# Performance work log

Hardware: AMD Instinct MI355X
Metric: run time of the kernel (lower is better)

## Reference

```python
import jax, jax.numpy as jnp
import numpy as np
from jax import lax

CONF_THRESH = 0.65
NMS_THRESH = 0.55
EPS = 1e-16


def setup_inputs() -> dict:
    key = jax.random.key(0)
    x = jax.random.uniform(key, (8, 4096, 85), dtype=jnp.float32)
    return {"x": x}


def _xywh2xyxy(b):
    # b: [..., 4] center-x, center-y, w, h -> x1, y1, x2, y2
    cx, cy, w, h = b[..., 0], b[..., 1], b[..., 2], b[..., 3]
    return jnp.stack([cx - w / 2, cy - h / 2, cx + w / 2, cy + h / 2], axis=-1)


def _pairwise_iou(boxes):
    # boxes: [bs, N, 4] in xyxy -> iou: [bs, N, N]
    x1, y1, x2, y2 = boxes[..., 0], boxes[..., 1], boxes[..., 2], boxes[..., 3]
    ix1 = jnp.maximum(x1[:, :, None], x1[:, None, :])
    iy1 = jnp.maximum(y1[:, :, None], y1[:, None, :])
    ix2 = jnp.minimum(x2[:, :, None], x2[:, None, :])
    iy2 = jnp.minimum(y2[:, :, None], y2[:, None, :])
    inter = jnp.clip(ix2 - ix1, 0.0) * jnp.clip(iy2 - iy1, 0.0)
    area = (x2 - x1) * (y2 - y1)
    return inter / (area[:, :, None] + area[:, None, :] - inter + EPS)


def reference(x):
    # x: [bs, N, 5 + nC]
    bs, N, _ = x.shape
    obj = x[..., 4]
    valid = obj > CONF_THRESH                      # foreground filter
    boxes = _xywh2xyxy(x[..., :4])
    max_conf = jnp.max(x[..., 5:], axis=-1)        # per-box best class score
    cls_idx = jnp.argmax(x[..., 5:], axis=-1)

    # sort descending by class confidence (invalid boxes pushed to the end)
    sort_key = jnp.where(valid, max_conf, -jnp.inf)
    order = jnp.argsort(-sort_key, axis=1)         # [bs, N]
    boxes_s = jnp.take_along_axis(boxes, order[..., None], axis=1)
    obj_s = jnp.take_along_axis(obj, order, axis=1)
    conf_s = jnp.take_along_axis(max_conf, order, axis=1)
    cls_s = jnp.take_along_axis(cls_idx, order, axis=1)
    valid_s = jnp.take_along_axis(valid, order, axis=1)

    # candidate suppression matrix: same class AND IoU above threshold
    iou = _pairwise_iou(boxes_s)                   # [bs, N, N]
    same_cls = cls_s[:, :, None] == cls_s[:, None, :]
    sup_mat = (iou > NMS_THRESH) & same_cls        # [bs, N, N]

    # greedy sequential NMS over boxes in descending-score order
    def step(suppressed, xs):
        sup_row, vld, i = xs                       # sup_row: [bs, N], vld: [bs]
        keep_i = vld & ~suppressed[:, i]
        suppressed = suppressed | (keep_i[:, None] & sup_row)
        return suppressed, keep_i

    xs = (jnp.swapaxes(sup_mat, 0, 1), valid_s.T, jnp.arange(N))
    _, keeps = lax.scan(step, jnp.zeros((bs, N), dtype=bool), xs)
    keep = keeps.T                                 # [bs, N]

    # [batch_idx, x1, y1, x2, y2, p_obj, max_conf, cls_idx]; non-kept rows zeroed
    batch_idx = jnp.broadcast_to(
        jnp.arange(bs, dtype=x.dtype)[:, None, None], (bs, N, 1))
    preds = jnp.concatenate(
        [batch_idx, boxes_s, obj_s[..., None], conf_s[..., None],
         cls_s[..., None].astype(x.dtype)], axis=-1)  # [bs, N, 8]
    return preds * keep[..., None].astype(x.dtype)
```

## Files before the change

### kernel.cpp

```cpp
#include <hip/hip_runtime.h>

constexpr int BS = 8;
constexpr int N  = 4096;
constexpr int F  = 85;
constexpr int NC = 80;
constexpr float CONF_T = 0.65f;
constexpr float NMS_T  = 0.55f;
constexpr int MC   = 96;
constexpr int SEGR = 32;
constexpr int SEGS = N / SEGR;


__global__ __launch_bounds__(256) void prep_kernel(
        const float* __restrict__ x,
        unsigned long long* __restrict__ gkeys,
        float4* __restrict__ vbox,
        float2* __restrict__ vco,
        int* __restrict__ cntblk,
        float4* __restrict__ out) {
    __shared__ __align__(16) float sx[SEGR * F];
    __shared__ int wq[4];
    const int tid = threadIdx.x, blk = blockIdx.x;
    const int row0 = blk * SEGR;
    const int b = blk >> 7;
    const float4* src = (const float4*)(x + (size_t)row0 * F);
    float4* dst = (float4*)sx;
    constexpr int NV4 = SEGR * F / 4;
    for (int i = tid; i < NV4; i += 256) dst[i] = src[i];
    if (tid < SEGR * 2)
        out[(size_t)row0 * 2 + tid] = make_float4(0.f, 0.f, 0.f, 0.f);
    __syncthreads();

    const int r = tid >> 3, h = tid & 7;
    float best; int bidx;
    {
        const float* p = sx + r * F + 5 + h * 10;
        float bv = p[0]; int bi = 0;
        #pragma unroll
        for (int c = 1; c < 10; ++c) {
            float v = p[c];
            if (v > bv) { bv = v; bi = c; }
        }
        best = bv; bidx = bi + h * 10;
    }
    #pragma unroll
    for (int d = 1; d < 8; d <<= 1) {
        float ov = __shfl_xor(best, d);
        int   oi = __shfl_xor(bidx, d);
        if (ov > best || (ov == best && oi < bidx)) { best = ov; bidx = oi; }
    }

    bool valid = false;
    unsigned long long key = 0;
    if (h == 0) {
        const float* p = sx + r * F;
        float obj = p[4];
        valid = obj > CONF_T;
        const int t = row0 + r;
        if (valid) {
            float cx = p[0], cy = p[1], w = p[2], hh = p[3];
            vbox[t] = make_float4(cx - w * 0.5f, cy - hh * 0.5f,
                                  cx + w * 0.5f, cy + hh * 0.5f);
            vco[t]  = make_float2(obj, best);
            key = ((unsigned long long)(~__float_as_uint(best)) << 19)
                | ((unsigned long long)(unsigned)(t & (N - 1)) << 7)
                | (unsigned)bidx;
        }
    }
    const int lane = tid & 63, w = tid >> 6;
    unsigned long long mask = __ballot(valid);
    if (lane == 0) wq[w] = __popcll(mask);
    __syncthreads();
    int base = 0;
    for (int i = 0; i < w; ++i) base += wq[i];
    if (valid) {
        int slot = base + __popcll(mask & ((1ull << lane) - 1ull));
        gkeys[((size_t)b << 12) + ((blk & (SEGS - 1)) << 5) + slot] = key;
    }
    if (tid == 0) cntblk[blk] = wq[0] + wq[1] + wq[2] + wq[3];
}

__global__ __launch_bounds__(256) void rank_kernel(
        const unsigned long long* __restrict__ gkeys,
        const float4* __restrict__ vbox,
        const float2* __restrict__ vco,
        const int* __restrict__ cntblk,
        float4* __restrict__ rbox,
        float2* __restrict__ rco,
        int* __restrict__ rcls,
        int* __restrict__ cnt) {
    __shared__ __align__(16) unsigned long long sk[N + 2];
    __shared__ int scnt[SEGS];
    __shared__ int soff[SEGS];
    __shared__ int snv;
    __shared__ int part[256];
    const int b = blockIdx.y, tid = threadIdx.x;
    if (tid < 64) {
        int v0 = cntblk[b * SEGS + 2 * tid];
        int v1 = cntblk[b * SEGS + 2 * tid + 1];
        int s = v0 + v1;
        int xx = s;
        #pragma unroll
        for (int d = 1; d < 64; d <<= 1) {
            int y = __shfl_up(xx, d);
            if (tid >= d) xx += y;
        }
        int excl = xx - s;
        scnt[2 * tid] = v0;  scnt[2 * tid + 1] = v1;
        soff[2 * tid] = excl; soff[2 * tid + 1] = excl + v0;
        if (tid == 63) snv = xx;
    }
    __syncthreads();
    const int nv = snv;
    if (blockIdx.x == 0 && tid == 0) cnt[b] = nv;
    const int c0 = blockIdx.x * 64;
    if (c0 >= nv) return;

    const unsigned long long* kb = gkeys + ((size_t)b << 12);
    #pragma unroll 4
    for (int g = tid; g < SEGS * SEGR; g += 256) {
        int s = g >> 5, j = g & 31;
        if (j < scnt[s]) sk[soff[s] + j] = kb[g];
    }
    if (tid == 0) { sk[nv] = ~0ull; sk[nv + 1] = ~0ull; }
    __syncthreads();

    const int li = tid & 63, q = tid >> 6;
    const int bi = c0 + li;
    const bool active = bi < nv;
    const unsigned long long myk = active ? sk[bi] : 0;
    const int P = (nv + 1) >> 1;
    const int j0 = (P * q) >> 2, j1 = (P * (q + 1)) >> 2;
    const ulonglong2* skp = (const ulonglong2*)sk;
    int cr = 0;
    for (int j = j0; j < j1; ++j) {
        ulonglong2 kk = skp[j];
        cr += (kk.x < myk) ? 1 : 0;
        cr += (kk.y < myk) ? 1 : 0;
    }
    part[tid] = cr;
    __syncthreads();
    if (q == 0 && active) {
        int rank = part[li] + part[li + 64] + part[li + 128] + part[li + 192];
        int idx = (int)((myk >> 7) & (N - 1));
        int s = (b << 12) + idx;
        int d = (b << 12) + rank;
        rbox[d] = vbox[s];
        rco[d]  = vco[s];
        rcls[d] = (int)(myk & 127u);
    }
}

__global__ __launch_bounds__(64) void nms_kernel(
        const float4* __restrict__ rbox,
        const float2* __restrict__ rco,
        const int* __restrict__ rcls,
        const int* __restrict__ cnt,
        float4* __restrict__ out) {
    __shared__ float4 sbox[MC];
    __shared__ unsigned short srank[MC];
    __shared__ unsigned char srem[MC];
    const int c = blockIdx.x, b = blockIdx.y, lane = threadIdx.x;
    const int bN = b << 12;
    const int nv = cnt[b];
    constexpr int MAXCH = 32;

    int cv[MAXCH];
    #pragma unroll
    for (int ch = 0; ch < MAXCH; ++ch) {
        int rn = ch * 64 + lane;
        cv[ch] = rcls[bN + (rn < nv ? rn : 0)];
    }
    int n = 0;
    #pragma unroll
    for (int ch = 0; ch < MAXCH; ++ch) {
        int rn = ch * 64 + lane;
        bool member = (rn < nv) && (cv[ch] == c);
        unsigned long long mb = __ballot(member);
        if (member) {
            int pos = n + __popcll(mb & ((1ull << lane) - 1ull));
            if (pos < MC) srank[pos] = (unsigned short)rn;
        }
        n += __popcll(mb);
    }
    for (int base = MAXCH * 64; base < nv; base += 64) {
        int rn = base + lane;
        bool member = (rn < nv) && (rcls[bN + (rn < nv ? rn : 0)] == c);
        unsigned long long mb = __ballot(member);
        if (member) {
            int pos = n + __popcll(mb & ((1ull << lane) - 1ull));
            if (pos < MC) srank[pos] = (unsigned short)rn;
        }
        n += __popcll(mb);
    }
    if (n > MC) n = MC;
    const int m = n;

    for (int i = lane; i < m; i += 64) {
        sbox[i] = rbox[bN + srank[i]];
        srem[i] = 0;
    }

    for (int i = 0; i < m; ++i) {
        if (srem[i]) continue;
        float4 bi4 = sbox[i];
        float ai = (bi4.z - bi4.x) * (bi4.w - bi4.y);
        for (int j = i + 1 + lane; j < m; j += 64) {
            if (!srem[j]) {
                float4 bj = sbox[j];
                float ix1 = fmaxf(bi4.x, bj.x);
                float iy1 = fmaxf(bi4.y, bj.y);
                float ix2 = fminf(bi4.z, bj.z);
                float iy2 = fminf(bi4.w, bj.w);
                float inter = fmaxf(ix2 - ix1, 0.0f) * fmaxf(iy2 - iy1, 0.0f);
                float aj = (bj.z - bj.x) * (bj.w - bj.y);
                float iou = inter / (ai + aj - inter + 1e-16f);
                if (iou > NMS_T) srem[j] = 1;
            }
        }
    }
    for (int j = lane; j < m; j += 64) {
        if (!srem[j]) {
            int rr = srank[j];
            float4 bq = sbox[j];
            float2 oc = rco[bN + rr];
            float4* o = out + (size_t)(bN + rr) * 2;
            o[0] = make_float4((float)b, bq.x, bq.y, bq.z);
            o[1] = make_float4(bq.w, oc.x, oc.y, (float)c);
        }
    }
}

extern "C" void kernel_launch(void* const* d_in, const int* in_sizes, int n_in,
                              void* d_out, int out_size, void* d_ws, size_t ws_size,
                              hipStream_t stream) {
    const float* x = (const float*)d_in[0];
    float4* out = (float4*)d_out;

    char* ws = (char*)d_ws;
    size_t off = 0;
    auto alloc = [&](size_t bytes) { char* p = ws + off; off += (bytes + 255) & ~255ull; return p; };
    unsigned long long* gkeys = (unsigned long long*)alloc(BS * N * 8);
    float4* vbox = (float4*)alloc(BS * N * 16);
    float2* vco  = (float2*)alloc(BS * N * 8);
    int*    cntblk = (int*)alloc(BS * SEGS * 4);
    float4* rbox = (float4*)alloc(BS * N * 16);
    float2* rco  = (float2*)alloc(BS * N * 8);
    int*    rcls = (int*)alloc(BS * N * 4);
    int*    cnt  = (int*)alloc(BS * 4);

    prep_kernel<<<BS * N / SEGR, 256, 0, stream>>>(x, gkeys, vbox, vco, cntblk, out);
    rank_kernel<<<dim3(64, BS), 256, 0, stream>>>(gkeys, vbox, vco, cntblk,
                                                  rbox, rco, rcls, cnt);
    nms_kernel<<<dim3(NC, BS), 64, 0, stream>>>(rbox, rco, rcls, cnt, out);
}
```

Measured before the change: 90.64 us.

## Fuse rank and per-class NMS into one kernel computing ranks only for class members

Merges the global rank/scatter kernel and the per-class NMS kernel into a single kernel launched per (class, batch). Each block compacts the valid keys, picks out its class members and computes global ranks only for those members (at most 96) instead of ranking every valid box. Within-class order comes from comparing keys in shared memory. This removes one launch and the rbox/rco/rcls global round trip. In exchange, every class block reloads and compacts the full key array for its batch, which duplicates that work 80 times.

```diff
diff --git a/kernel.cpp b/kernel.cpp
--- a/kernel.cpp
+++ b/kernel.cpp
@@ -80,21 +80,26 @@
     if (tid == 0) cntblk[blk] = wq[0] + wq[1] + wq[2] + wq[3];
 }
 
-__global__ __launch_bounds__(256) void rank_kernel(
+__global__ __launch_bounds__(256) void cnms_kernel(
         const unsigned long long* __restrict__ gkeys,
         const float4* __restrict__ vbox,
         const float2* __restrict__ vco,
         const int* __restrict__ cntblk,
-        float4* __restrict__ rbox,
-        float2* __restrict__ rco,
-        int* __restrict__ rcls,
-        int* __restrict__ cnt) {
+        float4* __restrict__ out) {
     __shared__ __align__(16) unsigned long long sk[N + 2];
     __shared__ int scnt[SEGS];
     __shared__ int soff[SEGS];
-    __shared__ int snv;
-    __shared__ int part[256];
-    const int b = blockIdx.y, tid = threadIdx.x;
+    __shared__ int snv, sm;
+    __shared__ unsigned long long skm[MC];
+    __shared__ int2 spart[256];
+    __shared__ float4 sbox[MC];
+    __shared__ float2 sco[MC];
+    __shared__ int sgrk[MC];
+    __shared__ unsigned char srem[MC];
+    const int c = blockIdx.x, b = blockIdx.y, tid = threadIdx.x;
+    const int bN = b << 12;
+    const int li = tid & 63, q = tid >> 6;
+
     if (tid < 64) {
         int v0 = cntblk[b * SEGS + 2 * tid];
         int v1 = cntblk[b * SEGS + 2 * tid + 1];
@@ -112,121 +117,112 @@
     }
     __syncthreads();
     const int nv = snv;
-    if (blockIdx.x == 0 && tid == 0) cnt[b] = nv;
-    const int c0 = blockIdx.x * 64;
-    if (c0 >= nv) return;
 
     const unsigned long long* kb = gkeys + ((size_t)b << 12);
-    #pragma unroll 4
-    for (int g = tid; g < SEGS * SEGR; g += 256) {
-        int s = g >> 5, j = g & 31;
-        if (j < scnt[s]) sk[soff[s] + j] = kb[g];
+    #pragma unroll
+    for (int r = 0; r < 4; ++r) {
+        unsigned long long v[4]; int gg[4];
+        #pragma unroll
+        for (int qq = 0; qq < 4; ++qq) { gg[qq] = tid + (r * 4 + qq) * 256; v[qq] = kb[gg[qq]]; }
+        #pragma unroll
+        for (int qq = 0; qq < 4; ++qq) {
+            int s = gg[qq] >> 5, j = gg[qq] & 31;
+            if (j < scnt[s]) sk[soff[s] + j] = v[qq];
+        }
     }
     if (tid == 0) { sk[nv] = ~0ull; sk[nv + 1] = ~0ull; }
     __syncthreads();
 
-    const int li = tid & 63, q = tid >> 6;
-    const int bi = c0 + li;
-    const bool active = bi < nv;
-    const unsigned long long myk = active ? sk[bi] : 0;
+    if (tid < 64) {
+        int mcount = 0;
+        const int nch = (nv + 63) >> 6;
+        for (int rc = 0; rc < nch; ++rc) {
+            int j = (rc << 6) + tid;
+            unsigned long long k = sk[j];
+            bool member = (j < nv) && ((int)(k & 127u) == c);
+            unsigned long long mb = __ballot(member);
+            if (member) {
+                int pos = mcount + __popcll(mb & ((1ull << tid) - 1ull));
+                if (pos < MC) skm[pos] = k;
+            }
+            mcount += __popcll(mb);
+        }
+        if (tid == 0) sm = (mcount < MC) ? mcount : MC;
+    }
+    __syncthreads();
+    const int m = sm;
+    if (m == 0) return;
+
+    const unsigned long long mk0 = (li < m)      ? skm[li]      : ~0ull;
+    const unsigned long long mk1 = (64 + li < m) ? skm[64 + li] : ~0ull;
     const int P = (nv + 1) >> 1;
     const int j0 = (P * q) >> 2, j1 = (P * (q + 1)) >> 2;
     const ulonglong2* skp = (const ulonglong2*)sk;
-    int cr = 0;
-    for (int j = j0; j < j1; ++j) {
-        ulonglong2 kk = skp[j];
-        cr += (kk.x < myk) ? 1 : 0;
-        cr += (kk.y < myk) ? 1 : 0;
-    }
-    part[tid] = cr;
-    __syncthreads();
-    if (q == 0 && active) {
-        int rank = part[li] + part[li + 64] + part[li + 128] + part[li + 192];
-        int idx = (int)((myk >> 7) & (N - 1));
-        int s = (b << 12) + idx;
-        int d = (b << 12) + rank;
-        rbox[d] = vbox[s];
-        rco[d]  = vco[s];
-        rcls[d] = (int)(myk & 127u);
-    }
-}
-
-__global__ __launch_bounds__(64) void nms_kernel(
-        const float4* __restrict__ rbox,
-        const float2* __restrict__ rco,
-        const int* __restrict__ rcls,
-        const int* __restrict__ cnt,
-        float4* __restrict__ out) {
-    __shared__ float4 sbox[MC];
-    __shared__ unsigned short srank[MC];
-    __shared__ unsigned char srem[MC];
-    const int c = blockIdx.x, b = blockIdx.y, lane = threadIdx.x;
-    const int bN = b << 12;
-    const int nv = cnt[b];
-    constexpr int MAXCH = 32;
-
-    int cv[MAXCH];
-    #pragma unroll
-    for (int ch = 0; ch < MAXCH; ++ch) {
-        int rn = ch * 64 + lane;
-        cv[ch] = rcls[bN + (rn < nv ? rn : 0)];
-    }
-    int n = 0;
-    #pragma unroll
-    for (int ch = 0; ch < MAXCH; ++ch) {
-        int rn = ch * 64 + lane;
-        bool member = (rn < nv) && (cv[ch] == c);
-        unsigned long long mb = __ballot(member);
-        if (member) {
-            int pos = n + __popcll(mb & ((1ull << lane) - 1ull));
-            if (pos < MC) srank[pos] = (unsigned short)rn;
-        }
-        n += __popcll(mb);
-    }
-    for (int base = MAXCH * 64; base < nv; base += 64) {
-        int rn = base + lane;
-        bool member = (rn < nv) && (rcls[bN + (rn < nv ? rn : 0)] == c);
-        unsigned long long mb = __ballot(member);
-        if (member) {
-            int pos = n + __popcll(mb & ((1ull << lane) - 1ull));
-            if (pos < MC) srank[pos] = (unsigned short)rn;
-        }
-        n += __popcll(mb);
-    }
-    if (n > MC) n = MC;
-    const int m = n;
-
-    for (int i = lane; i < m; i += 64) {
-        sbox[i] = rbox[bN + srank[i]];
-        srem[i] = 0;
-    }
-
-    for (int i = 0; i < m; ++i) {
-        if (srem[i]) continue;
-        float4 bi4 = sbox[i];
-        float ai = (bi4.z - bi4.x) * (bi4.w - bi4.y);
-        for (int j = i + 1 + lane; j < m; j += 64) {
+    int cr0 = 0, cr1 = 0;
+    if (m > 64) {
+        for (int j = j0; j < j1; ++j) {
+            ulonglong2 kk = skp[j];
+            cr0 += (kk.x < mk0) + (kk.y < mk0);
+            cr1 += (kk.x < mk1) + (kk.y < mk1);
+        }
+    } else {
+        for (int j = j0; j < j1; ++j) {
+            ulonglong2 kk = skp[j];
+            cr0 += (kk.x < mk0) + (kk.y < mk0);
+        }
+    }
+    spart[tid] = make_int2(cr0, cr1);
+    __syncthreads();
+
+    if (tid < 64) {
+        if (li < m) {
+            int grk = spart[li].x + spart[64 + li].x
+                    + spart[128 + li].x + spart[192 + li].x;
+            int wrk = 0;
+            for (int i2 = 0; i2 < m; ++i2) wrk += (skm[i2] < mk0);
+            int idx = (int)((mk0 >> 7) & (N - 1));
+            sbox[wrk] = vbox[bN + idx];
+            sco[wrk]  = vco[bN + idx];
+            sgrk[wrk] = grk;
+            srem[wrk] = 0;
+        }
+        if (m > 64 && 64 + li < m) {
+            int grk = spart[li].y + spart[64 + li].y
+                    + spart[128 + li].y + spart[192 + li].y;
+            int wrk = 0;
+            for (int i2 = 0; i2 < m; ++i2) wrk += (skm[i2] < mk1);
+            int idx = (int)((mk1 >> 7) & (N - 1));
+            sbox[wrk] = vbox[bN + idx];
+            sco[wrk]  = vco[bN + idx];
+            sgrk[wrk] = grk;
+            srem[wrk] = 0;
+        }
+        for (int i = 0; i < m; ++i) {
+            if (srem[i]) continue;
+            float4 bi4 = sbox[i];
+            float ai = (bi4.z - bi4.x) * (bi4.w - bi4.y);
+            for (int j = i + 1 + li; j < m; j += 64) {
+                if (!srem[j]) {
+                    float4 bj = sbox[j];
+                    float ix1 = fmaxf(bi4.x, bj.x);
+                    float iy1 = fmaxf(bi4.y, bj.y);
+                    float ix2 = fminf(bi4.z, bj.z);
+                    float iy2 = fminf(bi4.w, bj.w);
+                    float inter = fmaxf(ix2 - ix1, 0.0f) * fmaxf(iy2 - iy1, 0.0f);
+                    float aj = (bj.z - bj.x) * (bj.w - bj.y);
+                    float iou = inter / (ai + aj - inter + 1e-16f);
+                    if (iou > NMS_T) srem[j] = 1;
+                }
+            }
+        }
+        for (int j = li; j < m; j += 64) {
             if (!srem[j]) {
-                float4 bj = sbox[j];
-                float ix1 = fmaxf(bi4.x, bj.x);
-                float iy1 = fmaxf(bi4.y, bj.y);
-                float ix2 = fminf(bi4.z, bj.z);
-                float iy2 = fminf(bi4.w, bj.w);
-                float inter = fmaxf(ix2 - ix1, 0.0f) * fmaxf(iy2 - iy1, 0.0f);
-                float aj = (bj.z - bj.x) * (bj.w - bj.y);
-                float iou = inter / (ai + aj - inter + 1e-16f);
-                if (iou > NMS_T) srem[j] = 1;
+                float4 bq = sbox[j];
+                float2 oc = sco[j];
+                float4* o = out + (size_t)(bN + sgrk[j]) * 2;
+                o[0] = make_float4((float)b, bq.x, bq.y, bq.z);
+                o[1] = make_float4(bq.w, oc.x, oc.y, (float)c);
             }
-        }
-    }
-    for (int j = lane; j < m; j += 64) {
-        if (!srem[j]) {
-            int rr = srank[j];
-            float4 bq = sbox[j];
-            float2 oc = rco[bN + rr];
-            float4* o = out + (size_t)(bN + rr) * 2;
-            o[0] = make_float4((float)b, bq.x, bq.y, bq.z);
-            o[1] = make_float4(bq.w, oc.x, oc.y, (float)c);
         }
     }
 }
@@ -244,13 +240,7 @@
     float4* vbox = (float4*)alloc(BS * N * 16);
     float2* vco  = (float2*)alloc(BS * N * 8);
     int*    cntblk = (int*)alloc(BS * SEGS * 4);
-    float4* rbox = (float4*)alloc(BS * N * 16);
-    float2* rco  = (float2*)alloc(BS * N * 8);
-    int*    rcls = (int*)alloc(BS * N * 4);
-    int*    cnt  = (int*)alloc(BS * 4);
 
     prep_kernel<<<BS * N / SEGR, 256, 0, stream>>>(x, gkeys, vbox, vco, cntblk, out);
-    rank_kernel<<<dim3(64, BS), 256, 0, stream>>>(gkeys, vbox, vco, cntblk,
-                                                  rbox, rco, rcls, cnt);
-    nms_kernel<<<dim3(NC, BS), 64, 0, stream>>>(rbox, rco, rcls, cnt, out);
+    cnms_kernel<<<dim3(NC, BS), 256, 0, stream>>>(gkeys, vbox, vco, cntblk, out);
 }
```

Measured after the change: 87.79 us. -3.1%, faster.
